# Optimization experiments

Hardware: AMD Instinct MI355X
Metric: run time of the kernel (lower is better)

## Reference

```python
import jax, jax.numpy as jnp
import numpy as np


def setup_inputs() -> dict:
    key = jax.random.key(0)
    ks = jax.random.split(key, 5)
    N, d_in, d_out, H, T = 65536, 256, 256, 8, 256
    values = jax.random.normal(ks[0], (N, d_in), jnp.float32)
    w_qkv = jax.random.normal(ks[1], (3 * d_out, d_in), jnp.float32) / np.sqrt(d_in)
    b_qkv = jax.random.normal(ks[2], (3 * d_out,), jnp.float32) * 0.01
    w_lin = jax.random.normal(ks[3], (d_out, d_out), jnp.float32) / np.sqrt(d_out)
    b_lin = jax.random.normal(ks[4], (d_out,), jnp.float32) * 0.01
    # Sorted track ids with equal-length tracks (L = N // T observations each).
    track_ids = jnp.repeat(jnp.arange(T, dtype=jnp.int32), N // T)
    return dict(values=values, w_qkv=w_qkv, b_qkv=b_qkv, w_lin=w_lin,
                b_lin=b_lin, track_ids=track_ids, n_tracks=T, num_heads=H)


def reference(values, w_qkv, b_qkv, w_lin, b_lin, track_ids, n_tracks, num_heads):
    N, d_in = values.shape
    d_out = w_qkv.shape[0] // 3
    H = num_heads
    Dh = d_out // H
    L = N // n_tracks  # static max track length (tracks are equal-length here)

    # lin_qkv over all points at once: [N, 3*d_out] -> [N, 3, H, Dh]
    qkv = (values @ w_qkv.T + b_qkv).reshape(N, 3, H, Dh)

    # Position of each point within its (sorted) track segment.
    counts = jax.ops.segment_sum(jnp.ones(N, jnp.int32), track_ids, num_segments=n_tracks)
    starts = jnp.cumsum(counts) - counts  # exclusive prefix sum
    pos = jnp.arange(N, dtype=jnp.int32) - starts[track_ids]

    # Scatter into padded per-track layout: [T, L, 3, H, Dh]
    padded = jnp.zeros((n_tracks, L, 3, H, Dh), values.dtype).at[track_ids, pos].set(qkv)
    q = jnp.transpose(padded[:, :, 0], (0, 2, 1, 3))  # [T, H, L, Dh]
    k = jnp.transpose(padded[:, :, 1], (0, 2, 1, 3))
    v = jnp.transpose(padded[:, :, 2], (0, 2, 1, 3))

    scores = jnp.einsum('thld,thmd->thlm', q, k) / np.sqrt(Dh).astype(values.dtype)
    probs = jax.nn.softmax(scores, axis=-1)
    ctx = jnp.einsum('thlm,thmd->thld', probs, v)           # [T, H, L, Dh]
    ctx = jnp.transpose(ctx, (0, 2, 1, 3)).reshape(n_tracks, L, d_out)

    # Gather back to flat point order (equals torch's track-sorted concat order).
    new_values = ctx[track_ids, pos] @ w_lin.T + b_lin      # [N, d_out]
    return new_values
```

## Files before the change

kernel.cpp:

```cpp
#include <hip/hip_runtime.h>
#include <hip/hip_bf16.h>


typedef __attribute__((ext_vector_type(8))) short short8;
typedef __attribute__((ext_vector_type(4))) float f32x4;

__device__ __forceinline__ unsigned short f2bf(float f) {
    union { float f; unsigned int i; } c; c.f = f;
    unsigned int lsb = (c.i >> 16) & 1u;
    return (unsigned short)((c.i + 0x7fffu + lsb) >> 16);
}
__device__ __forceinline__ unsigned short f2bfn(float f) {
    union { __hip_bfloat16 h; unsigned short u; } c;
    c.h = __float2bfloat16(f);
    return c.u;
}
__device__ __forceinline__ short8 pack_bf8(f32x4 lo, f32x4 hi) {
    short8 r;
    r[0] = (short)f2bf(lo[0]); r[1] = (short)f2bf(lo[1]);
    r[2] = (short)f2bf(lo[2]); r[3] = (short)f2bf(lo[3]);
    r[4] = (short)f2bf(hi[0]); r[5] = (short)f2bf(hi[1]);
    r[6] = (short)f2bf(hi[2]); r[7] = (short)f2bf(hi[3]);
    return r;
}
__device__ __forceinline__ short8 loadB8(const unsigned short* p) { return *(const short8*)p; }
__device__ __forceinline__ short8 loadB8(const float* p) {
    return pack_bf8(*(const f32x4*)p, *(const f32x4*)(p + 4));
}
__device__ __forceinline__ void glds16(const unsigned short* g, unsigned short* l) {
    __builtin_amdgcn_global_load_lds(
        (const __attribute__((address_space(1))) unsigned int*)g,
        (__attribute__((address_space(3))) unsigned int*)l, 16, 0, 0);
}

__global__ __launch_bounds__(256)
void cvt_all(const float* __restrict__ values, const float* __restrict__ wqkv,
             const float* __restrict__ wlin, unsigned short* __restrict__ abf,
             unsigned short* __restrict__ wb, int na8, int do_w)
{
    const int i = blockIdx.x * 256 + threadIdx.x;
    if (i < na8) {
        const f32x4* p = (const f32x4*)values + (size_t)i * 2;
        *(short8*)(abf + (size_t)i * 8) = pack_bf8(p[0], p[1]);
    } else if (do_w) {
        const int j = i - na8;
        if (j < 32768) {
            const float* src = (j < 24576) ? wqkv + (size_t)j * 8
                                           : wlin + (size_t)(j - 24576) * 8;
            const f32x4* p = (const f32x4*)src;
            *(short8*)(wb + (size_t)j * 8) = pack_bf8(p[0], p[1]);
        }
    }
}

template <typename BT>
__global__ __launch_bounds__(256)
void gemm1_k(const unsigned short* __restrict__ A, const BT* __restrict__ Bt,
             const float* __restrict__ bias, unsigned short* __restrict__ qkvb,
             float qs)
{
    constexpr bool BF = (sizeof(BT) == 2);
    __shared__ __align__(16) unsigned short As[128 * 64];
    __shared__ __align__(16) unsigned short Bs[128 * 64];
    const int tid  = threadIdx.x;
    const int lane = tid & 63;
    const int wave = tid >> 6;
    const int wm = wave >> 1, wn = wave & 1;
    const int blk = blockIdx.x, sg = blk / 48, id = blk % 48;
    const int bm = sg * 8 + (id & 7), bn = id >> 3;
    const int fr = lane & 15, quad = lane >> 4;
    const int lr  = lane >> 3;
    const int lc8 = (lane & 7) * 8;

    f32x4 zz = {0.f, 0.f, 0.f, 0.f};
    f32x4 acc[4][4];
#pragma unroll
    for (int i = 0; i < 4; ++i)
#pragma unroll
        for (int j = 0; j < 4; ++j) acc[i][j] = zz;

    const unsigned short* Ab = A + (size_t)(bm * 128 + lr) * 256 + lc8;

    for (int k0 = 0; k0 < 256; k0 += 64) {
        short8 bv[4];
        if constexpr (!BF) {
#pragma unroll
            for (int i = 0; i < 4; ++i)
                bv[i] = loadB8(Bt + (size_t)(bn * 128 + (tid >> 3) + 32 * i) * 256 + k0 + (tid & 7) * 8);
        }
        __syncthreads();
#pragma unroll
        for (int i = 0; i < 4; ++i) {
            const int r0 = i * 32 + wave * 8;
            glds16(Ab + (size_t)r0 * 256 + k0, &As[r0 * 64]);
            if constexpr (BF)
                glds16((const unsigned short*)Bt + (size_t)(bn * 128 + r0 + lr) * 256 + k0 + lc8,
                       &Bs[r0 * 64]);
        }
        if constexpr (!BF) {
#pragma unroll
            for (int i = 0; i < 4; ++i)
                *(short8*)&Bs[((tid >> 3) + 32 * i) * 64 + (tid & 7) * 8] = bv[i];
        }
        __syncthreads();
#pragma unroll
        for (int kk = 0; kk < 2; ++kk) {
            short8 a[4], b[4];
            const int qa8 = (kk * 4 + quad) * 8;
#pragma unroll
            for (int f = 0; f < 4; ++f) {
                a[f] = *(const short8*)&As[(wm * 64 + f * 16 + fr) * 64 + qa8];
                b[f] = *(const short8*)&Bs[(wn * 64 + f * 16 + fr) * 64 + qa8];
            }
#pragma unroll
            for (int fm = 0; fm < 4; ++fm)
#pragma unroll
                for (int fn = 0; fn < 4; ++fn)
                    acc[fm][fn] = __builtin_amdgcn_mfma_f32_16x16x32_bf16(
                        a[fm], b[fn], acc[fm][fn], 0, 0, 0);
        }
    }
#pragma unroll
    for (int fn = 0; fn < 4; ++fn) {
        const int col = bn * 128 + wn * 64 + fn * 16 + fr;
        const int w = col >> 8, h = (col >> 5) & 7, d = col & 31;
        const float bv2 = bias[col];
        const float s = (col < 256) ? qs : 1.0f;
#pragma unroll
        for (int fm = 0; fm < 4; ++fm) {
            const int row0 = bm * 128 + wm * 64 + fm * 16 + quad * 4;
#pragma unroll
            for (int r = 0; r < 4; ++r) {
                const int row = row0 + r;
                const int t = row >> 8, l = row & 255;
                qkvb[(size_t)(((t * 8 + h) * 3 + w)) * 8192 + l * 32 + d] =
                    f2bf((acc[fm][fn][r] + bv2) * s);
            }
        }
    }
}

template <typename BT>
__global__ __launch_bounds__(256)
void gemm2_k(const unsigned short* __restrict__ qkvb, const BT* __restrict__ Bt,
             const float* __restrict__ bias, float* __restrict__ C)
{
    constexpr bool BF = (sizeof(BT) == 2);
    __shared__ __align__(16) unsigned short As[128 * 64];
    __shared__ __align__(16) unsigned short Bs[128 * 64];
    const int tid  = threadIdx.x;
    const int lane = tid & 63;
    const int wave = tid >> 6;
    const int wm = wave >> 1, wn = wave & 1;
    const int blk = blockIdx.x, sg = blk / 16, id = blk % 16;
    const int bm = sg * 8 + (id & 7), bn = id >> 3;
    const int fr = lane & 15, quad = lane >> 4;
    const int lr  = lane >> 3;
    const int lc8 = (lane & 7) * 8;
    const int t = bm >> 1;
    const int lbase = (bm & 1) * 128;

    f32x4 zz = {0.f, 0.f, 0.f, 0.f};
    f32x4 acc[4][4];
#pragma unroll
    for (int i = 0; i < 4; ++i)
#pragma unroll
        for (int j = 0; j < 4; ++j) acc[i][j] = zz;

    for (int k0 = 0; k0 < 256; k0 += 64) {
        const int kc = k0 + lc8;
        const int h = kc >> 5, rem = kc & 31;
        const unsigned short* Ab = qkvb + (size_t)((t * 8 + h) * 3) * 8192
                                   + (size_t)(lbase + lr) * 32 + rem;
        short8 bv[4];
        if constexpr (!BF) {
#pragma unroll
            for (int i = 0; i < 4; ++i)
                bv[i] = loadB8(Bt + (size_t)(bn * 128 + (tid >> 3) + 32 * i) * 256 + k0 + (tid & 7) * 8);
        }
        __syncthreads();
#pragma unroll
        for (int i = 0; i < 4; ++i) {
            const int r0 = i * 32 + wave * 8;
            glds16(Ab + (size_t)r0 * 32, &As[r0 * 64]);
            if constexpr (BF)
                glds16((const unsigned short*)Bt + (size_t)(bn * 128 + r0 + lr) * 256 + k0 + lc8,
                       &Bs[r0 * 64]);
        }
        if constexpr (!BF) {
#pragma unroll
            for (int i = 0; i < 4; ++i)
                *(short8*)&Bs[((tid >> 3) + 32 * i) * 64 + (tid & 7) * 8] = bv[i];
        }
        __syncthreads();
#pragma unroll
        for (int kk = 0; kk < 2; ++kk) {
            short8 a[4], b[4];
            const int qa8 = (kk * 4 + quad) * 8;
#pragma unroll
            for (int f = 0; f < 4; ++f) {
                a[f] = *(const short8*)&As[(wm * 64 + f * 16 + fr) * 64 + qa8];
                b[f] = *(const short8*)&Bs[(wn * 64 + f * 16 + fr) * 64 + qa8];
            }
#pragma unroll
            for (int fm = 0; fm < 4; ++fm)
#pragma unroll
                for (int fn = 0; fn < 4; ++fn)
                    acc[fm][fn] = __builtin_amdgcn_mfma_f32_16x16x32_bf16(
                        a[fm], b[fn], acc[fm][fn], 0, 0, 0);
        }
    }
#pragma unroll
    for (int fn = 0; fn < 4; ++fn) {
        const int col = bn * 128 + wn * 64 + fn * 16 + fr;
        const float bv2 = bias[col];
#pragma unroll
        for (int fm = 0; fm < 4; ++fm) {
            const int row0 = bm * 128 + wm * 64 + fm * 16 + quad * 4;
#pragma unroll
            for (int r = 0; r < 4; ++r)
                C[(size_t)(row0 + r) * 256 + col] = acc[fm][fn][r] + bv2;
        }
    }
}

__global__ __launch_bounds__(256, 4)
void attn_kernel(unsigned short* __restrict__ qkvb)
{
    __shared__ __align__(16) unsigned short vT[32 * 264];
    __shared__ __align__(16) unsigned short pbuf[4 * 2 * 16 * 20];
    const int tid = threadIdx.x, lane = tid & 63, wave = tid >> 6;
    const int t = blockIdx.x >> 3, h = blockIdx.x & 7;
    const int fr = lane & 15, quad = lane >> 4;
    const size_t baseQ = (size_t)((t * 8 + h) * 3) * 8192;
    const size_t baseK = baseQ + 8192;
    const size_t baseV = baseQ + 16384;

    {
        const unsigned short* vp = qkvb + baseV + (size_t)tid * 32;
        short8 v0 = *(const short8*)(vp);
        short8 v1 = *(const short8*)(vp + 8);
        short8 v2 = *(const short8*)(vp + 16);
        short8 v3 = *(const short8*)(vp + 24);
#pragma unroll
        for (int d = 0; d < 8; ++d) {
            vT[(d     ) * 264 + tid] = (unsigned short)v0[d];
            vT[(d +  8) * 264 + tid] = (unsigned short)v1[d];
            vT[(d + 16) * 264 + tid] = (unsigned short)v2[d];
            vT[(d + 24) * 264 + tid] = (unsigned short)v3[d];
        }
    }
    short8 qf[4];
#pragma unroll
    for (int fm = 0; fm < 4; ++fm)
        qf[fm] = *(const short8*)(qkvb + baseQ + (size_t)(wave * 64 + fm * 16 + fr) * 32 + quad * 8);

    __syncthreads();

    f32x4 zz = {0.f, 0.f, 0.f, 0.f};
    f32x4 O[4][2];
    float lsum[4][4];
#pragma unroll
    for (int fm = 0; fm < 4; ++fm) {
        O[fm][0] = zz; O[fm][1] = zz;
#pragma unroll
        for (int rg = 0; rg < 4; ++rg) lsum[fm][rg] = 0.f;
    }

    unsigned short* pw = pbuf + wave * (2 * 16 * 20);

    for (int jb = 0; jb < 4; ++jb) {
        const int j0 = jb * 64;
        short8 kf[4];
#pragma unroll
        for (int fn = 0; fn < 4; ++fn)
            kf[fn] = *(const short8*)(qkvb + baseK + (size_t)(j0 + fn * 16 + fr) * 32 + quad * 8);

#pragma unroll
        for (int fm = 0; fm < 4; ++fm) {
            f32x4 S[4];
            __builtin_amdgcn_s_setprio(1);
#pragma unroll
            for (int fn = 0; fn < 4; ++fn)
                S[fn] = __builtin_amdgcn_mfma_f32_16x16x32_bf16(
                    qf[fm], kf[fn], zz, 0, 0, 0);
            __builtin_amdgcn_s_setprio(0);

#pragma unroll
            for (int kb = 0; kb < 2; ++kb) {
#pragma unroll
                for (int rg = 0; rg < 4; ++rg) {
                    const int prow = quad * 4 + rg;
                    const float p0 = __builtin_amdgcn_exp2f(S[2 * kb    ][rg]);
                    const float p1 = __builtin_amdgcn_exp2f(S[2 * kb + 1][rg]);
                    lsum[fm][rg] += p0 + p1;
                    pw[          prow * 20 + fr] = f2bfn(p0);
                    pw[16 * 20 + prow * 20 + fr] = f2bfn(p1);
                }
                short8 pf = *(const short8*)&pw[(quad >> 1) * (16 * 20)
                                                + fr * 20 + (quad & 1) * 8];
                short8 vf[2];
#pragma unroll
                for (int fd = 0; fd < 2; ++fd)
                    vf[fd] = *(const short8*)&vT[(fd * 16 + fr) * 264 + j0 + kb * 32 + quad * 8];
                __builtin_amdgcn_s_setprio(1);
                O[fm][0] = __builtin_amdgcn_mfma_f32_16x16x32_bf16(pf, vf[0], O[fm][0], 0, 0, 0);
                O[fm][1] = __builtin_amdgcn_mfma_f32_16x16x32_bf16(pf, vf[1], O[fm][1], 0, 0, 0);
                __builtin_amdgcn_s_setprio(0);
            }
        }
    }

#pragma unroll
    for (int fm = 0; fm < 4; ++fm)
#pragma unroll
        for (int rg = 0; rg < 4; ++rg) {
            float l = lsum[fm][rg];
#pragma unroll
            for (int m = 8; m >= 1; m >>= 1) l += __shfl_xor(l, m, 64);
            lsum[fm][rg] = 1.0f / l;
        }
#pragma unroll
    for (int fm = 0; fm < 4; ++fm)
#pragma unroll
        for (int fd = 0; fd < 2; ++fd)
#pragma unroll
            for (int rg = 0; rg < 4; ++rg) {
                const int row = wave * 64 + fm * 16 + quad * 4 + rg;
                const int col = fd * 16 + fr;
                qkvb[baseQ + (size_t)row * 32 + col] = f2bfn(O[fm][fd][rg] * lsum[fm][rg]);
            }
}

extern "C" void kernel_launch(void* const* d_in, const int* in_sizes, int n_in,
                              void* d_out, int out_size, void* d_ws, size_t ws_size,
                              hipStream_t stream) {
    const float* values = (const float*)d_in[0];
    const float* w_qkv  = (const float*)d_in[1];
    const float* b_qkv  = (const float*)d_in[2];
    const float* w_lin  = (const float*)d_in[3];
    const float* b_lin  = (const float*)d_in[4];
    float* out = (float*)d_out;

    const int N = in_sizes[0] / 256;
    const float sc = 0.17677669529663687f * 1.4426950408889634f;
    unsigned short* qkvb = (unsigned short*)d_ws;
    const size_t qkvb_elems = (size_t)N * 768;
    unsigned short* abf = (unsigned short*)d_out;
    unsigned short* wb  = qkvb + qkvb_elems;
    const int wfit = (ws_size >= (qkvb_elems + 262144) * 2) ? 1 : 0;
    const int na8 = N * 256 / 8;

    cvt_all<<<dim3((na8 + (wfit ? 32768 : 0) + 255) / 256), 256, 0, stream>>>(
        values, w_qkv, w_lin, abf, wb, na8, wfit);
    if (wfit) {
        gemm1_k<unsigned short><<<dim3(3072), 256, 0, stream>>>(abf, wb, b_qkv, qkvb, sc);
        attn_kernel<<<dim3(2048), 256, 0, stream>>>(qkvb);
        gemm2_k<unsigned short><<<dim3(1024), 256, 0, stream>>>(qkvb, wb + 196608, b_lin, out);
    } else {
        gemm1_k<float><<<dim3(3072), 256, 0, stream>>>(abf, w_qkv, b_qkv, qkvb, sc);
        attn_kernel<<<dim3(2048), 256, 0, stream>>>(qkvb);
        gemm2_k<float><<<dim3(1024), 256, 0, stream>>>(qkvb, w_lin, b_lin, out);
    }
}
```

Baseline: 247.3 us.

## Write V transposed from QKV GEMM epilogue and load it directly in attention

The QKV projection epilogue now stores V in a d-major (transposed) layout. The attention kernel can then read V fragments straight from global memory into registers, so the shared-memory transpose stage and its block barrier go away. The cost is strided, less coalesced stores in the GEMM epilogue for V columns, plus V reloaded from global/L2 by every wave rather than staged once per block.

```diff
diff --git a/kernel.cpp b/kernel.cpp
--- a/kernel.cpp
+++ b/kernel.cpp
@@ -133,8 +133,10 @@
             for (int r = 0; r < 4; ++r) {
                 const int row = row0 + r;
                 const int t = row >> 8, l = row & 255;
-                qkvb[(size_t)(((t * 8 + h) * 3 + w)) * 8192 + l * 32 + d] =
-                    f2bf((acc[fm][fn][r] + bv2) * s);
+                const size_t slot = (size_t)((t * 8 + h) * 3 + w) * 8192;
+                const size_t off = (w == 2) ? (size_t)(d * 256 + l)
+                                            : (size_t)(l * 32 + d);
+                qkvb[slot + off] = f2bf((acc[fm][fn][r] + bv2) * s);
             }
         }
     }
@@ -227,7 +229,6 @@
 __global__ __launch_bounds__(256, 4)
 void attn_kernel(unsigned short* __restrict__ qkvb)
 {
-    __shared__ __align__(16) unsigned short vT[32 * 264];
     __shared__ __align__(16) unsigned short pbuf[4 * 2 * 16 * 20];
     const int tid = threadIdx.x, lane = tid & 63, wave = tid >> 6;
     const int t = blockIdx.x >> 3, h = blockIdx.x & 7;
@@ -236,26 +237,10 @@
     const size_t baseK = baseQ + 8192;
     const size_t baseV = baseQ + 16384;
 
-    {
-        const unsigned short* vp = qkvb + baseV + (size_t)tid * 32;
-        short8 v0 = *(const short8*)(vp);
-        short8 v1 = *(const short8*)(vp + 8);
-        short8 v2 = *(const short8*)(vp + 16);
-        short8 v3 = *(const short8*)(vp + 24);
-#pragma unroll
-        for (int d = 0; d < 8; ++d) {
-            vT[(d     ) * 264 + tid] = (unsigned short)v0[d];
-            vT[(d +  8) * 264 + tid] = (unsigned short)v1[d];
-            vT[(d + 16) * 264 + tid] = (unsigned short)v2[d];
-            vT[(d + 24) * 264 + tid] = (unsigned short)v3[d];
-        }
-    }
     short8 qf[4];
 #pragma unroll
     for (int fm = 0; fm < 4; ++fm)
         qf[fm] = *(const short8*)(qkvb + baseQ + (size_t)(wave * 64 + fm * 16 + fr) * 32 + quad * 8);
-
-    __syncthreads();
 
     f32x4 zz = {0.f, 0.f, 0.f, 0.f};
     f32x4 O[4][2];
@@ -275,6 +260,13 @@
 #pragma unroll
         for (int fn = 0; fn < 4; ++fn)
             kf[fn] = *(const short8*)(qkvb + baseK + (size_t)(j0 + fn * 16 + fr) * 32 + quad * 8);
+        short8 vg[2][2];
+#pragma unroll
+        for (int kb = 0; kb < 2; ++kb)
+#pragma unroll
+            for (int fd = 0; fd < 2; ++fd)
+                vg[kb][fd] = *(const short8*)(qkvb + baseV
+                                + (size_t)(fd * 16 + fr) * 256 + j0 + kb * 32 + quad * 8);
 
 #pragma unroll
         for (int fm = 0; fm < 4; ++fm) {
@@ -299,13 +291,9 @@
                 }
                 short8 pf = *(const short8*)&pw[(quad >> 1) * (16 * 20)
                                                 + fr * 20 + (quad & 1) * 8];
-                short8 vf[2];
-#pragma unroll
-                for (int fd = 0; fd < 2; ++fd)
-                    vf[fd] = *(const short8*)&vT[(fd * 16 + fr) * 264 + j0 + kb * 32 + quad * 8];
                 __builtin_amdgcn_s_setprio(1);
-                O[fm][0] = __builtin_amdgcn_mfma_f32_16x16x32_bf16(pf, vf[0], O[fm][0], 0, 0, 0);
-                O[fm][1] = __builtin_amdgcn_mfma_f32_16x16x32_bf16(pf, vf[1], O[fm][1], 0, 0, 0);
+                O[fm][0] = __builtin_amdgcn_mfma_f32_16x16x32_bf16(pf, vg[kb][0], O[fm][0], 0, 0, 0);
+                O[fm][1] = __builtin_amdgcn_mfma_f32_16x16x32_bf16(pf, vg[kb][1], O[fm][1], 0, 0, 0);
                 __builtin_amdgcn_s_setprio(0);
             }
         }
```

Result: slower. 279.2 us (+12.9%).
